# Kernel tuning notes

Hardware: AMD Instinct MI355X
Metric: run time of the kernel (lower is better)

Reference implementation:

```python
import jax, jax.numpy as jnp
import numpy as np

B, L, QD, KVD, H = 8, 1024, 1024, 768, 16
DH = QD // H
EPS = 1e-5


def setup_inputs() -> dict:
    key = jax.random.key(0)
    ks = jax.random.split(key, 12)
    q = jax.random.normal(ks[0], (B, L, QD), jnp.float32)
    k = jax.random.normal(ks[1], (B, L, KVD), jnp.float32)
    v = jax.random.normal(ks[2], (B, L, KVD), jnp.float32)
    # key_padding_mask: True = valid token (code masks where ~mask)
    lengths = jax.random.randint(ks[3], (B,), L // 2, L + 1)
    key_padding_mask = jnp.arange(L)[None, :] < lengths[:, None]
    def lin(kk, fan_in, fan_out):
        bound = 1.0 / np.sqrt(fan_in)
        k1, k2 = jax.random.split(kk)
        W = jax.random.uniform(k1, (fan_out, fan_in), jnp.float32, -bound, bound)
        b = jax.random.uniform(k2, (fan_out,), jnp.float32, -bound, bound)
        return W, b
    Wq, bq = lin(ks[4], QD, QD)
    Wk, bk = lin(ks[5], KVD, QD)
    Wv, bv = lin(ks[6], KVD, QD)
    Wo, bo = lin(ks[7], QD, QD)
    gamma = jnp.ones((QD,), jnp.float32)
    beta = jnp.zeros((QD,), jnp.float32)
    return {"q": q, "k": k, "v": v, "key_padding_mask": key_padding_mask,
            "Wq": Wq, "bq": bq, "Wk": Wk, "bk": bk, "Wv": Wv, "bv": bv,
            "Wo": Wo, "bo": bo, "gamma": gamma, "beta": beta}


def reference(q, k, v, key_padding_mask, Wq, bq, Wk, bk, Wv, bv, Wo, bo, gamma, beta):
    Bq, Lq, C = q.shape
    scale = DH ** -0.5
    # projections -> [B, H, L, DH]
    qh = (q @ Wq.T + bq).reshape(Bq, Lq, H, DH).transpose(0, 2, 1, 3)
    kh = (k @ Wk.T + bk).reshape(Bq, Lq, H, DH).transpose(0, 2, 1, 3)
    vh = (v @ Wv.T + bv).reshape(Bq, Lq, H, DH).transpose(0, 2, 1, 3)
    attn = jnp.einsum('bhld,bhmd->bhlm', qh, kh) * scale
    attn = jnp.where(key_padding_mask[:, None, None, :], attn, -jnp.inf)
    p = jax.nn.softmax(attn, axis=-1)
    out = jnp.einsum('bhlm,bhmd->bhld', p, vh).transpose(0, 2, 1, 3).reshape(Bq, Lq, C)
    out = out @ Wo.T + bo  # dropout is identity in eval
    y = out + q
    mu = jnp.mean(y, axis=-1, keepdims=True)
    var = jnp.var(y, axis=-1, keepdims=True)
    return (y - mu) * jax.lax.rsqrt(var + EPS) * gamma + beta
```

## Files before the change

kernel.cpp:

```cpp
#include <hip/hip_runtime.h>
#include <stdint.h>

typedef float f32x4 __attribute__((ext_vector_type(4)));
typedef __bf16 bf16x8 __attribute__((ext_vector_type(8)));
typedef unsigned short u16;

__device__ __forceinline__ void gload_lds16(const void* g, void* l) {
  __builtin_amdgcn_global_load_lds(
      (__attribute__((address_space(1))) void*)(uintptr_t)(g),
      (__attribute__((address_space(3))) void*)(uint32_t)(uintptr_t)(l),
      16, 0, 0);
}

__device__ __forceinline__ u16 f2bf(float x) {
  __bf16 h = (__bf16)x;
  return *(u16*)&h;
}

__device__ __forceinline__ void barrier_raw() {
  __builtin_amdgcn_sched_barrier(0);
  __builtin_amdgcn_s_barrier();
  __builtin_amdgcn_sched_barrier(0);
}

__global__ __launch_bounds__(256) void cast_all(
    const float* __restrict__ q, const float* __restrict__ k,
    const float* __restrict__ v, const float* __restrict__ wq,
    const float* __restrict__ wk, const float* __restrict__ wv,
    const float* __restrict__ wo, u16* __restrict__ out) {
  const int g = blockIdx.x;
  const float* in;
  int s;
  if (g < 8192) { in = q; s = 0; }
  else if (g < 14336) { in = k; s = 8192; }
  else if (g < 20480) { in = v; s = 14336; }
  else if (g < 21504) { in = wq; s = 20480; }
  else if (g < 22272) { in = wk; s = 21504; }
  else if (g < 23040) { in = wv; s = 22272; }
  else { in = wo; s = 23040; }
  const int li = (g - s) * 256 + threadIdx.x;
  float4 x = *((const float4*)in + li);
  unsigned lo = (unsigned)f2bf(x.x) | ((unsigned)f2bf(x.y) << 16);
  unsigned hi = (unsigned)f2bf(x.z) | ((unsigned)f2bf(x.w) << 16);
  ((uint2*)out)[(size_t)g * 256 + threadIdx.x] = make_uint2(lo, hi);
}

__global__ __launch_bounds__(256, 2) void proj_kernel(
    const u16* __restrict__ qb, const u16* __restrict__ kb,
    const u16* __restrict__ vb, const u16* __restrict__ wqb,
    const u16* __restrict__ wkb, const u16* __restrict__ wvb,
    const float* __restrict__ bq, const float* __restrict__ bk,
    const float* __restrict__ bv, u16* __restrict__ qpb,
    u16* __restrict__ kpb, u16* __restrict__ vtb) {
  __shared__ __align__(16) u16 As[3][256 * 32];
  __shared__ __align__(16) u16 Bs[3][128 * 32];
  const int tid = threadIdx.x;
  const int role = blockIdx.y >> 3;
  const int m0 = blockIdx.x * 256, n0 = (blockIdx.y & 7) * 128;
  const int K = (role == 0) ? 1024 : 768;
  const u16* A = (role == 0) ? qb : ((role == 1) ? kb : vb);
  const u16* Bt = (role == 0) ? wqb : ((role == 1) ? wkb : wvb);
  const float* bias = (role == 0) ? bq : ((role == 1) ? bk : bv);
  const int lane = tid & 63, w = tid >> 6;
  const int wr = w >> 1, wc = w & 1;
  const int l16 = lane & 15, lk = lane >> 4;
  const int nk = K >> 5;
  const int srow = tid >> 2;
  const int sw = (tid & 3) ^ ((tid >> 3) & 3);

  const u16* Ap = A + (size_t)(m0 + srow) * K + sw * 8;
  const u16* Bp = Bt + (size_t)(n0 + srow) * K + sw * 8;

  f32x4 acc[8][4] = {};

  auto stage = [&](int t, int ko) {
#pragma unroll
    for (int l = 0; l < 4; ++l)
      gload_lds16(Ap + (size_t)l * 64 * K + ko, As[t] + tid * 8 + l * 2048);
#pragma unroll
    for (int l = 0; l < 2; ++l)
      gload_lds16(Bp + (size_t)l * 64 * K + ko, Bs[t] + tid * 8 + l * 2048);
  };

  stage(0, 0);
  stage(1, 32);

  const int e2 = (l16 >> 1) & 3;
  int cur = 0;
  for (int kt = 0; kt < nk; ++kt) {
    const int stg = (cur >= 1) ? cur - 1 : 2;
    if (kt + 2 < nk) {
      stage(stg, (kt + 2) << 5);
      asm volatile("s_waitcnt vmcnt(12)" ::: "memory");
    } else if (kt + 1 < nk) {
      asm volatile("s_waitcnt vmcnt(6)" ::: "memory");
    } else {
      asm volatile("s_waitcnt vmcnt(0)" ::: "memory");
    }
    barrier_raw();

    bf16x8 a[8], b[4];
#pragma unroll
    for (int i = 0; i < 8; ++i)
      a[i] = *(const bf16x8*)(As[cur] + (wr * 128 + i * 16 + l16) * 32 + (lk ^ e2) * 8);
#pragma unroll
    for (int j = 0; j < 4; ++j)
      b[j] = *(const bf16x8*)(Bs[cur] + (wc * 64 + j * 16 + l16) * 32 + (lk ^ e2) * 8);
    __builtin_amdgcn_s_setprio(1);
#pragma unroll
    for (int i = 0; i < 8; ++i)
#pragma unroll
      for (int j = 0; j < 4; ++j)
        acc[i][j] = __builtin_amdgcn_mfma_f32_16x16x32_bf16(a[i], b[j], acc[i][j], 0, 0, 0);
    __builtin_amdgcn_s_setprio(0);
    barrier_raw();
    cur = (cur < 2) ? cur + 1 : 0;
  }

#pragma unroll
  for (int i = 0; i < 8; ++i) {
    const int mrow = m0 + wr * 128 + i * 16 + lk * 4;
#pragma unroll
    for (int j = 0; j < 4; ++j) {
      const int col = n0 + wc * 64 + j * 16 + l16;
      const float bval = bias[col];
      if (role == 0) {
#pragma unroll
        for (int r = 0; r < 4; ++r)
          qpb[(size_t)(mrow + r) * 1024 + col] = f2bf(acc[i][j][r] + bval);
      } else if (role == 1) {
#pragma unroll
        for (int r = 0; r < 4; ++r)
          kpb[(size_t)(mrow + r) * 1024 + col] = f2bf(acc[i][j][r] + bval);
      } else {
        const int bb = mrow >> 10, l = mrow & 1023;
        const int hh = col >> 6, dd = col & 63;
        u16 u0 = f2bf(acc[i][j][0] + bval);
        u16 u1 = f2bf(acc[i][j][1] + bval);
        u16 u2 = f2bf(acc[i][j][2] + bval);
        u16 u3 = f2bf(acc[i][j][3] + bval);
        uint2 pkt = make_uint2((unsigned)u0 | ((unsigned)u1 << 16),
                               (unsigned)u2 | ((unsigned)u3 << 16));
        *(uint2*)(vtb + ((size_t)((bb * 16 + hh) * 64 + dd) << 10) + l) = pkt;
      }
    }
  }
}

__global__ __launch_bounds__(256) void attn_kernel(
    const u16* __restrict__ qp, const u16* __restrict__ kp,
    const u16* __restrict__ vt, const int* __restrict__ mask,
    u16* __restrict__ out) {
  __shared__ __align__(16) u16 KV[2][2][64 * 64];
  __shared__ __align__(16) u16 Ps[4][16 * 64];
  const int tid = threadIdx.x;
  const int qt = blockIdx.x, h = blockIdx.y, b = blockIdx.z;
  const int lane = tid & 63, w = tid >> 6;
  const int l16 = lane & 15, lk = lane >> 4;
  const int srow = tid >> 3, schunk = tid & 7;
  const int sw = schunk ^ (srow & 7);

  int cnt = 0;
  {
    const int4* mp = (const int4*)(mask + (b << 10));
#pragma unroll
    for (int i = 0; i < 4; ++i) {
      const int4 mv = mp[lane * 4 + i];
      cnt += (mv.x ? 1 : 0) + (mv.y ? 1 : 0) + (mv.z ? 1 : 0) + (mv.w ? 1 : 0);
    }
#pragma unroll
    for (int off = 1; off < 64; off <<= 1) cnt += __shfl_xor(cnt, off);
  }
  const int ntile = (cnt + 63) >> 6;
  const int rem = cnt & 63;

#pragma unroll
  for (int p = 0; p < 2; ++p) {
    gload_lds16(qp + (((size_t)(b * 1024 + qt * 64 + p * 32 + srow)) << 10) + h * 64 + sw * 8,
                KV[1][0] + tid * 8 + p * 2048);
    gload_lds16(kp + (((size_t)(b * 1024 + p * 32 + srow)) << 10) + h * 64 + sw * 8,
                KV[0][0] + tid * 8 + p * 2048);
    gload_lds16(vt + (((size_t)((b * 16 + h) * 64 + p * 32 + srow)) << 10) + sw * 8,
                KV[0][1] + tid * 8 + p * 2048);
  }
  __syncthreads();
  const int qrow = w * 16 + l16, qs = qrow & 7;
  bf16x8 aq0 = *(const bf16x8*)(KV[1][0] + qrow * 64 + (lk ^ qs) * 8);
  bf16x8 aq1 = *(const bf16x8*)(KV[1][0] + qrow * 64 + ((lk + 4) ^ qs) * 8);
  __syncthreads();

  const float SC2 = 0.18033688011112042f;
  float lsumq = 0.f;
  f32x4 oacc[4] = {};
  const int e7 = l16 & 7;

  int cur = 0;
  for (int kt = 0; kt < ntile; ++kt) {
    if (kt + 1 < ntile) {
#pragma unroll
      for (int p = 0; p < 2; ++p) {
        gload_lds16(kp + (((size_t)(b * 1024 + (kt + 1) * 64 + p * 32 + srow)) << 10) + h * 64 + sw * 8,
                    KV[cur ^ 1][0] + tid * 8 + p * 2048);
        gload_lds16(vt + (((size_t)((b * 16 + h) * 64 + p * 32 + srow)) << 10) + (kt + 1) * 64 + sw * 8,
                    KV[cur ^ 1][1] + tid * 8 + p * 2048);
      }
    }
    const u16* Kb = KV[cur][0];
    const u16* Vb = KV[cur][1];

    f32x4 sfr[4] = {};
    __builtin_amdgcn_s_setprio(1);
#pragma unroll
    for (int nf = 0; nf < 4; ++nf) {
      const int krow = nf * 16 + l16;
      bf16x8 bk0 = *(const bf16x8*)(Kb + krow * 64 + (lk ^ e7) * 8);
      bf16x8 bk1 = *(const bf16x8*)(Kb + krow * 64 + ((lk + 4) ^ e7) * 8);
      sfr[nf] = __builtin_amdgcn_mfma_f32_16x16x32_bf16(bk0, aq0, sfr[nf], 0, 0, 0);
      sfr[nf] = __builtin_amdgcn_mfma_f32_16x16x32_bf16(bk1, aq1, sfr[nf], 0, 0, 0);
    }
    __builtin_amdgcn_s_setprio(0);

    const bool partial = (kt == ntile - 1) && (rem != 0);
    u16* Pw = &Ps[w][0];
#pragma unroll
    for (int nf = 0; nf < 4; ++nf) {
      float pv0 = __builtin_amdgcn_exp2f(sfr[nf][0] * SC2);
      float pv1 = __builtin_amdgcn_exp2f(sfr[nf][1] * SC2);
      float pv2 = __builtin_amdgcn_exp2f(sfr[nf][2] * SC2);
      float pv3 = __builtin_amdgcn_exp2f(sfr[nf][3] * SC2);
      if (partial) {
        const int k0 = nf * 16 + lk * 4;
        pv0 = (k0 + 0 < rem) ? pv0 : 0.f;
        pv1 = (k0 + 1 < rem) ? pv1 : 0.f;
        pv2 = (k0 + 2 < rem) ? pv2 : 0.f;
        pv3 = (k0 + 3 < rem) ? pv3 : 0.f;
      }
      lsumq += (pv0 + pv1) + (pv2 + pv3);
      unsigned lo = (unsigned)f2bf(pv0) | ((unsigned)f2bf(pv1) << 16);
      unsigned hi = (unsigned)f2bf(pv2) | ((unsigned)f2bf(pv3) << 16);
      *(uint2*)(Pw + l16 * 64 + (((nf * 2 + (lk >> 1)) ^ e7) * 8 + (lk & 1) * 4)) =
          make_uint2(lo, hi);
    }

    bf16x8 ap0 = *(const bf16x8*)(Pw + l16 * 64 + ((lk ^ e7) * 8));
    bf16x8 ap1 = *(const bf16x8*)(Pw + l16 * 64 + (((4 + lk) ^ e7) * 8));
    __builtin_amdgcn_s_setprio(1);
#pragma unroll
    for (int nf = 0; nf < 4; ++nf) {
      const int vrow = nf * 16 + l16;
      bf16x8 bv0 = *(const bf16x8*)(Vb + vrow * 64 + (lk ^ e7) * 8);
      bf16x8 bv1 = *(const bf16x8*)(Vb + vrow * 64 + ((lk + 4) ^ e7) * 8);
      oacc[nf] = __builtin_amdgcn_mfma_f32_16x16x32_bf16(ap0, bv0, oacc[nf], 0, 0, 0);
      oacc[nf] = __builtin_amdgcn_mfma_f32_16x16x32_bf16(ap1, bv1, oacc[nf], 0, 0, 0);
    }
    __builtin_amdgcn_s_setprio(0);

    __syncthreads();
    cur ^= 1;
  }

  lsumq += __shfl_xor(lsumq, 16);
  lsumq += __shfl_xor(lsumq, 32);
  float rinv[4];
#pragma unroll
  for (int r = 0; r < 4; ++r) rinv[r] = 1.0f / __shfl(lsumq, lk * 4 + r);

#pragma unroll
  for (int nf = 0; nf < 4; ++nf)
#pragma unroll
    for (int r = 0; r < 4; ++r) {
      const int tok = b * 1024 + qt * 64 + w * 16 + lk * 4 + r;
      const int col = h * 64 + nf * 16 + l16;
      out[((size_t)tok << 10) + col] = f2bf(oacc[nf][r] * rinv[r]);
    }
}

__global__ __launch_bounds__(256) void gemm_o(
    const u16* __restrict__ A, const u16* __restrict__ Bt,
    const float* __restrict__ bias, float* __restrict__ Cf,
    const float* __restrict__ res) {
  __shared__ __align__(16) u16 As[3][128 * 32];
  __shared__ __align__(16) u16 Bs[3][128 * 32];
  const int K = 1024, N = 1024, nk = 32;
  const int tid = threadIdx.x;
  const int m0 = blockIdx.x * 128, n0 = blockIdx.y * 128;
  const int lane = tid & 63, w = tid >> 6;
  const int wr = w >> 1, wc = w & 1;
  const int l16 = lane & 15, lk = lane >> 4;
  const int srow = tid >> 2;
  const int sw = (tid & 3) ^ ((tid >> 3) & 3);

  const u16* Ap = A + (size_t)(m0 + srow) * K + sw * 8;
  const u16* Bp = Bt + (size_t)(n0 + srow) * K + sw * 8;

  f32x4 acc[4][4] = {};

#pragma unroll
  for (int t = 0; t < 2; ++t)
#pragma unroll
    for (int p = 0; p < 2; ++p) {
      gload_lds16(Ap + (size_t)p * 64 * K + t * 32, As[t] + tid * 8 + p * 2048);
      gload_lds16(Bp + (size_t)p * 64 * K + t * 32, Bs[t] + tid * 8 + p * 2048);
    }

  const int e2 = (l16 >> 1) & 3;
  int cur = 0;
  for (int kt = 0; kt < nk; ++kt) {
    const int stg = (cur >= 1) ? cur - 1 : 2;
    if (kt + 2 < nk) {
      const int ko = (kt + 2) << 5;
#pragma unroll
      for (int p = 0; p < 2; ++p) {
        gload_lds16(Ap + (size_t)p * 64 * K + ko, As[stg] + tid * 8 + p * 2048);
        gload_lds16(Bp + (size_t)p * 64 * K + ko, Bs[stg] + tid * 8 + p * 2048);
      }
      asm volatile("s_waitcnt vmcnt(8)" ::: "memory");
    } else if (kt + 1 < nk) {
      asm volatile("s_waitcnt vmcnt(4)" ::: "memory");
    } else {
      asm volatile("s_waitcnt vmcnt(0)" ::: "memory");
    }
    barrier_raw();

    bf16x8 a[4], b[4];
#pragma unroll
    for (int i = 0; i < 4; ++i)
      a[i] = *(const bf16x8*)(As[cur] + (wr * 64 + i * 16 + l16) * 32 + (lk ^ e2) * 8);
#pragma unroll
    for (int j = 0; j < 4; ++j)
      b[j] = *(const bf16x8*)(Bs[cur] + (wc * 64 + j * 16 + l16) * 32 + (lk ^ e2) * 8);
    __builtin_amdgcn_s_setprio(1);
#pragma unroll
    for (int i = 0; i < 4; ++i)
#pragma unroll
      for (int j = 0; j < 4; ++j)
        acc[i][j] = __builtin_amdgcn_mfma_f32_16x16x32_bf16(a[i], b[j], acc[i][j], 0, 0, 0);
    __builtin_amdgcn_s_setprio(0);
    barrier_raw();
    cur = (cur < 2) ? cur + 1 : 0;
  }

#pragma unroll
  for (int i = 0; i < 4; ++i) {
    const int mrow = m0 + wr * 64 + i * 16 + lk * 4;
#pragma unroll
    for (int j = 0; j < 4; ++j) {
      const int col = n0 + wc * 64 + j * 16 + l16;
      const float bval = bias[col];
#pragma unroll
      for (int r = 0; r < 4; ++r) {
        const size_t idx = (size_t)(mrow + r) * N + col;
        Cf[idx] = acc[i][j][r] + bval + res[idx];
      }
    }
  }
}

__global__ __launch_bounds__(256) void ln_kernel(float* __restrict__ y,
                                                 const float* __restrict__ gamma,
                                                 const float* __restrict__ beta) {
  __shared__ float ssum[4], ssq[4];
  const int tid = threadIdx.x;
  float* yr = y + ((size_t)blockIdx.x << 10);
  float4 v = *((const float4*)yr + tid);
  float s = v.x + v.y + v.z + v.w;
  float q2 = v.x * v.x + v.y * v.y + v.z * v.z + v.w * v.w;
#pragma unroll
  for (int off = 1; off < 64; off <<= 1) {
    s += __shfl_xor(s, off);
    q2 += __shfl_xor(q2, off);
  }
  if ((tid & 63) == 0) { ssum[tid >> 6] = s; ssq[tid >> 6] = q2; }
  __syncthreads();
  s = ssum[0] + ssum[1] + ssum[2] + ssum[3];
  q2 = ssq[0] + ssq[1] + ssq[2] + ssq[3];
  const float mu = s * (1.0f / 1024.0f);
  const float rstd = rsqrtf(q2 * (1.0f / 1024.0f) - mu * mu + 1e-5f);
  float4 g = *((const float4*)gamma + tid);
  float4 be = *((const float4*)beta + tid);
  float4 o;
  o.x = (v.x - mu) * rstd * g.x + be.x;
  o.y = (v.y - mu) * rstd * g.y + be.y;
  o.z = (v.z - mu) * rstd * g.z + be.z;
  o.w = (v.w - mu) * rstd * g.w + be.w;
  *((float4*)yr + tid) = o;
}

extern "C" void kernel_launch(void* const* d_in, const int* in_sizes, int n_in,
                              void* d_out, int out_size, void* d_ws, size_t ws_size,
                              hipStream_t stream) {
  (void)in_sizes; (void)n_in; (void)out_size; (void)ws_size;
  const float* q = (const float*)d_in[0];
  const float* k = (const float*)d_in[1];
  const float* v = (const float*)d_in[2];
  const int* msk = (const int*)d_in[3];
  const float* Wq = (const float*)d_in[4];
  const float* bq = (const float*)d_in[5];
  const float* Wk = (const float*)d_in[6];
  const float* bk = (const float*)d_in[7];
  const float* Wv = (const float*)d_in[8];
  const float* bv = (const float*)d_in[9];
  const float* Wo = (const float*)d_in[10];
  const float* bo = (const float*)d_in[11];
  const float* gamma = (const float*)d_in[12];
  const float* beta = (const float*)d_in[13];
  float* out = (float*)d_out;

  char* p = (char*)d_ws;
  auto take = [&p](size_t bytes) {
    char* r = p;
    p += (bytes + 255) & ~(size_t)255;
    return r;
  };
  u16* qb = (u16*)take(8192ull * 1024 * 2);
  u16* kb = (u16*)take(8192ull * 768 * 2);
  u16* vb = (u16*)take(8192ull * 768 * 2);
  u16* wqb = (u16*)take(1024ull * 1024 * 2);
  u16* wkb = (u16*)take(1024ull * 768 * 2);
  u16* wvb = (u16*)take(1024ull * 768 * 2);
  u16* wob = (u16*)take(1024ull * 1024 * 2);
  u16* qpb = (u16*)take(8192ull * 1024 * 2);
  u16* kpb = (u16*)take(8192ull * 1024 * 2);
  u16* vtb = (u16*)take(8192ull * 1024 * 2);
  u16* atb = (u16*)take(8192ull * 1024 * 2);

  cast_all<<<dim3(24064), 256, 0, stream>>>(q, k, v, Wq, Wk, Wv, Wo, qb);

  proj_kernel<<<dim3(32, 24), 256, 0, stream>>>(qb, kb, vb, wqb, wkb, wvb,
                                                bq, bk, bv, qpb, kpb, vtb);

  attn_kernel<<<dim3(16, 16, 8), 256, 0, stream>>>(qpb, kpb, vtb, msk, atb);

  gemm_o<<<dim3(64, 8), 256, 0, stream>>>(atb, wob, bo, out, q);

  ln_kernel<<<dim3(8192), 256, 0, stream>>>(out, gamma, beta);
}
```

Measured before the change: 179.1 us.

## Double-buffer LDS fragment reads against MFMA in projection and output GEMMs

Restructures the K loops of the projection and output GEMMs into a 2-step unrolled pipeline. The LDS-to-register fragment reads for the next k-tile are issued while MFMAs run on the current tile's registers, which is meant to hide LDS read latency behind matrix math. The projection grid is reordered so Q/K/V roles interleave across blockIdx.y, and gemm_o gets a 3-blocks-per-SM launch bound. The change adds register pressure from the doubled fragment buffers and extra barriers per iteration.

```diff
diff --git a/kernel.cpp b/kernel.cpp
--- a/kernel.cpp
+++ b/kernel.cpp
@@ -22,6 +22,13 @@
   __builtin_amdgcn_s_barrier();
   __builtin_amdgcn_sched_barrier(0);
 }
+
+#define VMCNT(n) asm volatile("s_waitcnt vmcnt(" #n ")" ::: "memory")
+#define LGKM0()                                    \
+  do {                                             \
+    asm volatile("s_waitcnt lgkmcnt(0)" ::: "memory"); \
+    __builtin_amdgcn_sched_barrier(0);             \
+  } while (0)
 
 __global__ __launch_bounds__(256) void cast_all(
     const float* __restrict__ q, const float* __restrict__ k,
@@ -55,8 +62,8 @@
   __shared__ __align__(16) u16 As[3][256 * 32];
   __shared__ __align__(16) u16 Bs[3][128 * 32];
   const int tid = threadIdx.x;
-  const int role = blockIdx.y >> 3;
-  const int m0 = blockIdx.x * 256, n0 = (blockIdx.y & 7) * 128;
+  const int role = blockIdx.y % 3;
+  const int m0 = blockIdx.x * 256, n0 = (blockIdx.y / 3) * 128;
   const int K = (role == 0) ? 1024 : 768;
   const u16* A = (role == 0) ? qb : ((role == 1) ? kb : vb);
   const u16* Bt = (role == 0) ? wqb : ((role == 1) ? wkb : wvb);
@@ -67,13 +74,16 @@
   const int nk = K >> 5;
   const int srow = tid >> 2;
   const int sw = (tid & 3) ^ ((tid >> 3) & 3);
+  const int e2 = (l16 >> 1) & 3;
 
   const u16* Ap = A + (size_t)(m0 + srow) * K + sw * 8;
   const u16* Bp = Bt + (size_t)(n0 + srow) * K + sw * 8;
 
   f32x4 acc[8][4] = {};
-
-  auto stage = [&](int t, int ko) {
+  bf16x8 aA[8], bA[4], aB[8], bB[4];
+
+  auto stage = [&](int t, int ktile) {
+    const int ko = ktile << 5;
 #pragma unroll
     for (int l = 0; l < 4; ++l)
       gload_lds16(Ap + (size_t)l * 64 * K + ko, As[t] + tid * 8 + l * 2048);
@@ -81,31 +91,15 @@
     for (int l = 0; l < 2; ++l)
       gload_lds16(Bp + (size_t)l * 64 * K + ko, Bs[t] + tid * 8 + l * 2048);
   };
-
-  stage(0, 0);
-  stage(1, 32);
-
-  const int e2 = (l16 >> 1) & 3;
-  int cur = 0;
-  for (int kt = 0; kt < nk; ++kt) {
-    const int stg = (cur >= 1) ? cur - 1 : 2;
-    if (kt + 2 < nk) {
-      stage(stg, (kt + 2) << 5);
-      asm volatile("s_waitcnt vmcnt(12)" ::: "memory");
-    } else if (kt + 1 < nk) {
-      asm volatile("s_waitcnt vmcnt(6)" ::: "memory");
-    } else {
-      asm volatile("s_waitcnt vmcnt(0)" ::: "memory");
-    }
-    barrier_raw();
-
-    bf16x8 a[8], b[4];
+  auto rd = [&](bf16x8 (&a)[8], bf16x8 (&b)[4], int c) {
 #pragma unroll
     for (int i = 0; i < 8; ++i)
-      a[i] = *(const bf16x8*)(As[cur] + (wr * 128 + i * 16 + l16) * 32 + (lk ^ e2) * 8);
+      a[i] = *(const bf16x8*)(As[c] + (wr * 128 + i * 16 + l16) * 32 + (lk ^ e2) * 8);
 #pragma unroll
     for (int j = 0; j < 4; ++j)
-      b[j] = *(const bf16x8*)(Bs[cur] + (wc * 64 + j * 16 + l16) * 32 + (lk ^ e2) * 8);
+      b[j] = *(const bf16x8*)(Bs[c] + (wc * 64 + j * 16 + l16) * 32 + (lk ^ e2) * 8);
+  };
+  auto mm = [&](bf16x8 (&a)[8], bf16x8 (&b)[4]) {
     __builtin_amdgcn_s_setprio(1);
 #pragma unroll
     for (int i = 0; i < 8; ++i)
@@ -113,8 +107,34 @@
       for (int j = 0; j < 4; ++j)
         acc[i][j] = __builtin_amdgcn_mfma_f32_16x16x32_bf16(a[i], b[j], acc[i][j], 0, 0, 0);
     __builtin_amdgcn_s_setprio(0);
-    barrier_raw();
-    cur = (cur < 2) ? cur + 1 : 0;
+  };
+
+  stage(0, 0);
+  stage(1, 1);
+  VMCNT(6);
+  barrier_raw();
+  rd(aA, bA, 0);
+  LGKM0();
+
+  int cur = 0;
+  for (int kt = 0; kt < nk; kt += 2) {
+    const int c1 = (cur == 2) ? 0 : cur + 1;
+    const int c2 = (c1 == 2) ? 0 : c1 + 1;
+    if (kt + 2 < nk) { stage(c2, kt + 2); VMCNT(6); }
+    else { VMCNT(0); }
+    barrier_raw();
+    rd(aB, bB, c1);
+    mm(aA, bA);
+    LGKM0();
+    barrier_raw();
+    if (kt + 3 < nk) { stage(cur, kt + 3); VMCNT(6); }
+    else { VMCNT(0); }
+    barrier_raw();
+    if (kt + 2 < nk) rd(aA, bA, c2);
+    mm(aB, bB);
+    LGKM0();
+    barrier_raw();
+    cur = c2;
   }
 
 #pragma unroll
@@ -275,7 +295,7 @@
     }
 }
 
-__global__ __launch_bounds__(256) void gemm_o(
+__global__ __launch_bounds__(256, 3) void gemm_o(
     const u16* __restrict__ A, const u16* __restrict__ Bt,
     const float* __restrict__ bias, float* __restrict__ Cf,
     const float* __restrict__ res) {
@@ -289,46 +309,31 @@
   const int l16 = lane & 15, lk = lane >> 4;
   const int srow = tid >> 2;
   const int sw = (tid & 3) ^ ((tid >> 3) & 3);
+  const int e2 = (l16 >> 1) & 3;
 
   const u16* Ap = A + (size_t)(m0 + srow) * K + sw * 8;
   const u16* Bp = Bt + (size_t)(n0 + srow) * K + sw * 8;
 
   f32x4 acc[4][4] = {};
-
-#pragma unroll
-  for (int t = 0; t < 2; ++t)
+  bf16x8 aA[4], bA[4], aB[4], bB[4];
+
+  auto stage = [&](int t, int ktile) {
+    const int ko = ktile << 5;
 #pragma unroll
     for (int p = 0; p < 2; ++p) {
-      gload_lds16(Ap + (size_t)p * 64 * K + t * 32, As[t] + tid * 8 + p * 2048);
-      gload_lds16(Bp + (size_t)p * 64 * K + t * 32, Bs[t] + tid * 8 + p * 2048);
-    }
-
-  const int e2 = (l16 >> 1) & 3;
-  int cur = 0;
-  for (int kt = 0; kt < nk; ++kt) {
-    const int stg = (cur >= 1) ? cur - 1 : 2;
-    if (kt + 2 < nk) {
-      const int ko = (kt + 2) << 5;
-#pragma unroll
-      for (int p = 0; p < 2; ++p) {
-        gload_lds16(Ap + (size_t)p * 64 * K + ko, As[stg] + tid * 8 + p * 2048);
-        gload_lds16(Bp + (size_t)p * 64 * K + ko, Bs[stg] + tid * 8 + p * 2048);
-      }
-      asm volatile("s_waitcnt vmcnt(8)" ::: "memory");
-    } else if (kt + 1 < nk) {
-      asm volatile("s_waitcnt vmcnt(4)" ::: "memory");
-    } else {
-      asm volatile("s_waitcnt vmcnt(0)" ::: "memory");
-    }
-    barrier_raw();
-
-    bf16x8 a[4], b[4];
+      gload_lds16(Ap + (size_t)p * 64 * K + ko, As[t] + tid * 8 + p * 2048);
+      gload_lds16(Bp + (size_t)p * 64 * K + ko, Bs[t] + tid * 8 + p * 2048);
+    }
+  };
+  auto rd = [&](bf16x8 (&a)[4], bf16x8 (&b)[4], int c) {
 #pragma unroll
     for (int i = 0; i < 4; ++i)
-      a[i] = *(const bf16x8*)(As[cur] + (wr * 64 + i * 16 + l16) * 32 + (lk ^ e2) * 8);
+      a[i] = *(const bf16x8*)(As[c] + (wr * 64 + i * 16 + l16) * 32 + (lk ^ e2) * 8);
 #pragma unroll
     for (int j = 0; j < 4; ++j)
-      b[j] = *(const bf16x8*)(Bs[cur] + (wc * 64 + j * 16 + l16) * 32 + (lk ^ e2) * 8);
+      b[j] = *(const bf16x8*)(Bs[c] + (wc * 64 + j * 16 + l16) * 32 + (lk ^ e2) * 8);
+  };
+  auto mm = [&](bf16x8 (&a)[4], bf16x8 (&b)[4]) {
     __builtin_amdgcn_s_setprio(1);
 #pragma unroll
     for (int i = 0; i < 4; ++i)
@@ -336,8 +341,34 @@
       for (int j = 0; j < 4; ++j)
         acc[i][j] = __builtin_amdgcn_mfma_f32_16x16x32_bf16(a[i], b[j], acc[i][j], 0, 0, 0);
     __builtin_amdgcn_s_setprio(0);
-    barrier_raw();
-    cur = (cur < 2) ? cur + 1 : 0;
+  };
+
+  stage(0, 0);
+  stage(1, 1);
+  VMCNT(4);
+  barrier_raw();
+  rd(aA, bA, 0);
+  LGKM0();
+
+  int cur = 0;
+  for (int kt = 0; kt < nk; kt += 2) {
+    const int c1 = (cur == 2) ? 0 : cur + 1;
+    const int c2 = (c1 == 2) ? 0 : c1 + 1;
+    if (kt + 2 < nk) { stage(c2, kt + 2); VMCNT(4); }
+    else { VMCNT(0); }
+    barrier_raw();
+    rd(aB, bB, c1);
+    mm(aA, bA);
+    LGKM0();
+    barrier_raw();
+    if (kt + 3 < nk) { stage(cur, kt + 3); VMCNT(4); }
+    else { VMCNT(0); }
+    barrier_raw();
+    if (kt + 2 < nk) rd(aA, bA, c2);
+    mm(aB, bB);
+    LGKM0();
+    barrier_raw();
+    cur = c2;
   }
 
 #pragma unroll
```

Measured after the change: 202.1 us. 12.8% more time.

## Use one barrier per k-step in GEMMs and remap attention blocks by head

Applied to the files above, without the earlier changes.

Both GEMM main loops now wait on the current stage and barrier once at the top, then issue the prefetch for stage kt+2 into the buffer consumed last iteration. This drops the second barrier per k-step. The triple buffer keeps the overwrite safe, because every wave has passed the top barrier before anyone writes that slot. The attention launch becomes a 1D grid whose index is decoded so consecutive blocks cover 8 batch-head pairs for the same query tile, which changes L2/cache locality and the order in which blocks reach the CUs. gemm_o also gets a minimum-occupancy hint of 3 blocks per CU, which may constrain register allocation.

```diff
diff --git a/kernel.cpp b/kernel.cpp
--- a/kernel.cpp
+++ b/kernel.cpp
@@ -22,6 +22,8 @@
   __builtin_amdgcn_s_barrier();
   __builtin_amdgcn_sched_barrier(0);
 }
+
+#define VMCNT(n) asm volatile("s_waitcnt vmcnt(" #n ")" ::: "memory")
 
 __global__ __launch_bounds__(256) void cast_all(
     const float* __restrict__ q, const float* __restrict__ k,
@@ -88,17 +90,12 @@
   const int e2 = (l16 >> 1) & 3;
   int cur = 0;
   for (int kt = 0; kt < nk; ++kt) {
-    const int stg = (cur >= 1) ? cur - 1 : 2;
+    if (kt + 1 < nk) { VMCNT(6); } else { VMCNT(0); }
+    barrier_raw();
     if (kt + 2 < nk) {
+      const int stg = (cur >= 1) ? cur - 1 : 2;
       stage(stg, (kt + 2) << 5);
-      asm volatile("s_waitcnt vmcnt(12)" ::: "memory");
-    } else if (kt + 1 < nk) {
-      asm volatile("s_waitcnt vmcnt(6)" ::: "memory");
-    } else {
-      asm volatile("s_waitcnt vmcnt(0)" ::: "memory");
-    }
-    barrier_raw();
-
+    }
     bf16x8 a[8], b[4];
 #pragma unroll
     for (int i = 0; i < 8; ++i)
@@ -113,7 +110,6 @@
       for (int j = 0; j < 4; ++j)
         acc[i][j] = __builtin_amdgcn_mfma_f32_16x16x32_bf16(a[i], b[j], acc[i][j], 0, 0, 0);
     __builtin_amdgcn_s_setprio(0);
-    barrier_raw();
     cur = (cur < 2) ? cur + 1 : 0;
   }
 
@@ -154,7 +150,10 @@
   __shared__ __align__(16) u16 KV[2][2][64 * 64];
   __shared__ __align__(16) u16 Ps[4][16 * 64];
   const int tid = threadIdx.x;
-  const int qt = blockIdx.x, h = blockIdx.y, b = blockIdx.z;
+  const int bid = blockIdx.x;
+  const int qt = (bid >> 3) & 15;
+  const int bh = (bid & 7) + ((bid >> 7) << 3);
+  const int b = bh >> 4, h = bh & 15;
   const int lane = tid & 63, w = tid >> 6;
   const int l16 = lane & 15, lk = lane >> 4;
   const int srow = tid >> 3, schunk = tid & 7;
@@ -275,7 +274,7 @@
     }
 }
 
-__global__ __launch_bounds__(256) void gemm_o(
+__global__ __launch_bounds__(256, 3) void gemm_o(
     const u16* __restrict__ A, const u16* __restrict__ Bt,
     const float* __restrict__ bias, float* __restrict__ Cf,
     const float* __restrict__ res) {
@@ -289,39 +288,32 @@
   const int l16 = lane & 15, lk = lane >> 4;
   const int srow = tid >> 2;
   const int sw = (tid & 3) ^ ((tid >> 3) & 3);
+  const int e2 = (l16 >> 1) & 3;
 
   const u16* Ap = A + (size_t)(m0 + srow) * K + sw * 8;
   const u16* Bp = Bt + (size_t)(n0 + srow) * K + sw * 8;
 
   f32x4 acc[4][4] = {};
 
-#pragma unroll
-  for (int t = 0; t < 2; ++t)
+  auto stage = [&](int t, int ko) {
 #pragma unroll
     for (int p = 0; p < 2; ++p) {
-      gload_lds16(Ap + (size_t)p * 64 * K + t * 32, As[t] + tid * 8 + p * 2048);
-      gload_lds16(Bp + (size_t)p * 64 * K + t * 32, Bs[t] + tid * 8 + p * 2048);
-    }
-
-  const int e2 = (l16 >> 1) & 3;
+      gload_lds16(Ap + (size_t)p * 64 * K + ko, As[t] + tid * 8 + p * 2048);
+      gload_lds16(Bp + (size_t)p * 64 * K + ko, Bs[t] + tid * 8 + p * 2048);
+    }
+  };
+
+  stage(0, 0);
+  stage(1, 32);
+
   int cur = 0;
   for (int kt = 0; kt < nk; ++kt) {
-    const int stg = (cur >= 1) ? cur - 1 : 2;
+    if (kt + 1 < nk) { VMCNT(4); } else { VMCNT(0); }
+    barrier_raw();
     if (kt + 2 < nk) {
-      const int ko = (kt + 2) << 5;
-#pragma unroll
-      for (int p = 0; p < 2; ++p) {
-        gload_lds16(Ap + (size_t)p * 64 * K + ko, As[stg] + tid * 8 + p * 2048);
-        gload_lds16(Bp + (size_t)p * 64 * K + ko, Bs[stg] + tid * 8 + p * 2048);
-      }
-      asm volatile("s_waitcnt vmcnt(8)" ::: "memory");
-    } else if (kt + 1 < nk) {
-      asm volatile("s_waitcnt vmcnt(4)" ::: "memory");
-    } else {
-      asm volatile("s_waitcnt vmcnt(0)" ::: "memory");
-    }
-    barrier_raw();
-
+      const int stg = (cur >= 1) ? cur - 1 : 2;
+      stage(stg, (kt + 2) << 5);
+    }
     bf16x8 a[4], b[4];
 #pragma unroll
     for (int i = 0; i < 4; ++i)
@@ -336,7 +328,6 @@
       for (int j = 0; j < 4; ++j)
         acc[i][j] = __builtin_amdgcn_mfma_f32_16x16x32_bf16(a[i], b[j], acc[i][j], 0, 0, 0);
     __builtin_amdgcn_s_setprio(0);
-    barrier_raw();
     cur = (cur < 2) ? cur + 1 : 0;
   }
 
@@ -429,7 +420,7 @@
   proj_kernel<<<dim3(32, 24), 256, 0, stream>>>(qb, kb, vb, wqb, wkb, wvb,
                                                 bq, bk, bv, qpb, kpb, vtb);
 
-  attn_kernel<<<dim3(16, 16, 8), 256, 0, stream>>>(qpb, kpb, vtb, msk, atb);
+  attn_kernel<<<dim3(2048), 256, 0, stream>>>(qpb, kpb, vtb, msk, atb);
 
   gemm_o<<<dim3(64, 8), 256, 0, stream>>>(atb, wob, bo, out, q);
 
```

Result: faster. 173.9 us (median of 2 runs) (-2.9%).
